# Optimization experiments

Measured on AMD Instinct MI355X. Metric: run time of the kernel, lower is better.

## Reference

```python
import jax, jax.numpy as jnp
import numpy as np
from jax import lax

IN, H, L, NC = 1024, 256, 3, 8
B, T = 64, 512


def setup_inputs() -> dict:
    key = jax.random.key(0)
    ks = iter(jax.random.split(key, 32))
    def u(shape, fan_in):
        s = 1.0 / np.sqrt(fan_in)
        return jax.random.uniform(next(ks), shape, jnp.float32, -s, s)
    inp = {"x": jax.random.normal(next(ks), (B, T, IN), jnp.float32)}
    dims = [IN, H, H]
    for l in range(L):
        inp[f"Wih{l}"] = u((4 * H, dims[l]), H)
        inp[f"Whh{l}"] = u((4 * H, H), H)
        # combined bias b_ih + b_hh (mathematically identical)
        inp[f"b{l}"] = u((4 * H,), H) + u((4 * H,), H)
    inp["W1"] = u((128, H), H)
    inp["bfc1"] = u((128,), H)
    inp["W2"] = u((NC, 128), 128)
    inp["bfc2"] = u((NC,), 128)
    return inp


def _lstm_layer(x_tbd, Wih, Whh, b):
    # x_tbd: (T, B, D). Precompute input gates with one big GEMM.
    xg = jnp.einsum("tbd,gd->tbg", x_tbd, Wih) + b  # (T, B, 4H)
    h0 = jnp.zeros((x_tbd.shape[1], H), x_tbd.dtype)
    def step(carry, xg_t):
        h, c = carry
        g = xg_t + h @ Whh.T
        i, f, gg, o = jnp.split(g, 4, axis=-1)  # torch gate order i,f,g,o
        i, f, o = jax.nn.sigmoid(i), jax.nn.sigmoid(f), jax.nn.sigmoid(o)
        c = f * c + i * jnp.tanh(gg)
        h = o * jnp.tanh(c)
        return (h, c), h
    _, hs = lax.scan(step, (h0, h0), xg)
    return hs  # (T, B, H)


def reference(x, Wih0, Whh0, b0, Wih1, Whh1, b1, Wih2, Whh2, b2, W1, bfc1, W2, bfc2):
    h = jnp.transpose(x, (1, 0, 2))  # (T, B, IN)
    for Wih, Whh, b in ((Wih0, Whh0, b0), (Wih1, Whh1, b1), (Wih2, Whh2, b2)):
        h = _lstm_layer(h, Wih, Whh, b)
    last = h[-1]  # (B, H) output at final timestep
    z = jax.nn.relu(last @ W1.T + bfc1)
    return z @ W2.T + bfc2  # (B, NC)
```

## Files before the change

### kernel.cpp

```cpp
#include <hip/hip_runtime.h>
#include <hip/hip_cooperative_groups.h>
#include <cmath>

namespace cg = cooperative_groups;

#define IN_DIM 1024
#define HD 256
#define G4H 1024
#define BB 64
#define TT 512
#define NCLS 8

#define SLOT_STRIDE (HD * BB)
#define LAYER_STRIDE (4 * SLOT_STRIDE)

__device__ __forceinline__ float sigmoidf_(float x) {
    return 1.0f / (1.0f + __expf(-x));
}
__device__ __forceinline__ float tanhf_(float x) {
    return 2.0f / (1.0f + __expf(-2.0f * x)) - 1.0f;
}
__device__ __forceinline__ unsigned long long ld_agent_u64(const unsigned long long* p) {
    return __hip_atomic_load(p, __ATOMIC_RELAXED, __HIP_MEMORY_SCOPE_AGENT);
}
__device__ __forceinline__ void st_agent_u64(unsigned long long* p, unsigned long long v) {
    __hip_atomic_store(p, v, __ATOMIC_RELAXED, __HIP_MEMORY_SCOPE_AGENT);
}

#define GBM 128
#define GBN 128
#define GBK 16

__global__ __launch_bounds__(256) void xg0_gemm(const float* __restrict__ x,
                                                const float* __restrict__ Wih0,
                                                const float* __restrict__ b0,
                                                float* __restrict__ xg0T) {
    __shared__ float As[GBK][GBM];
    __shared__ float Bs[GBK][GBN];
    const int m0 = blockIdx.y * GBM;
    const int n0 = blockIdx.x * GBN;
    const int tid = threadIdx.x;
    const int tx = tid & 15;
    const int ty = tid >> 4;
    const int lr = tid >> 1;
    const int lk = (tid & 1) * 8;
    const int am = m0 + lr;
    const size_t arow = (size_t)(am & 63) * TT + (am >> 6);
    float acc[8][8] = {};
    for (int k0 = 0; k0 < IN_DIM; k0 += GBK) {
        const float4 a0 = *(const float4*)&x[arow * IN_DIM + k0 + lk];
        const float4 a1 = *(const float4*)&x[arow * IN_DIM + k0 + lk + 4];
        const float4 w0 = *(const float4*)&Wih0[(size_t)(n0 + lr) * IN_DIM + k0 + lk];
        const float4 w1 = *(const float4*)&Wih0[(size_t)(n0 + lr) * IN_DIM + k0 + lk + 4];
        __syncthreads();
        As[lk + 0][lr] = a0.x; As[lk + 1][lr] = a0.y; As[lk + 2][lr] = a0.z; As[lk + 3][lr] = a0.w;
        As[lk + 4][lr] = a1.x; As[lk + 5][lr] = a1.y; As[lk + 6][lr] = a1.z; As[lk + 7][lr] = a1.w;
        Bs[lk + 0][lr] = w0.x; Bs[lk + 1][lr] = w0.y; Bs[lk + 2][lr] = w0.z; Bs[lk + 3][lr] = w0.w;
        Bs[lk + 4][lr] = w1.x; Bs[lk + 5][lr] = w1.y; Bs[lk + 6][lr] = w1.z; Bs[lk + 7][lr] = w1.w;
        __syncthreads();
#pragma unroll
        for (int k = 0; k < GBK; ++k) {
            const float4 av0 = *(const float4*)&As[k][ty * 8];
            const float4 av1 = *(const float4*)&As[k][ty * 8 + 4];
            const float4 bv0 = *(const float4*)&Bs[k][tx * 8];
            const float4 bv1 = *(const float4*)&Bs[k][tx * 8 + 4];
            const float am8[8] = {av0.x, av0.y, av0.z, av0.w, av1.x, av1.y, av1.z, av1.w};
            const float bn8[8] = {bv0.x, bv0.y, bv0.z, bv0.w, bv1.x, bv1.y, bv1.z, bv1.w};
#pragma unroll
            for (int i = 0; i < 8; ++i)
#pragma unroll
                for (int jj = 0; jj < 8; ++jj)
                    acc[i][jj] = fmaf(am8[i], bn8[jj], acc[i][jj]);
        }
    }
    const float4 bias0 = *(const float4*)&b0[n0 + tx * 8];
    const float4 bias1 = *(const float4*)&b0[n0 + tx * 8 + 4];
    const float bia[8] = {bias0.x, bias0.y, bias0.z, bias0.w, bias1.x, bias1.y, bias1.z, bias1.w};
#pragma unroll
    for (int i = 0; i < 8; ++i) {
        const int m = m0 + ty * 8 + i;
        const int t = m >> 6;
        const int bb = m & 63;
#pragma unroll
        for (int jj = 0; jj < 8; ++jj) {
            const int n = n0 + tx * 8 + jj;
            xg0T[((size_t)t * G4H + n) * BB + bb] = acc[i][jj] + bia[jj];
        }
    }
}

__global__ __launch_bounds__(512) void lstm_cells(
    const float* __restrict__ xg0T,
    const float* __restrict__ Whh0,
    const float* __restrict__ Wih1, const float* __restrict__ Whh1, const float* __restrict__ b1,
    const float* __restrict__ Wih2, const float* __restrict__ Whh2, const float* __restrict__ b2,
    unsigned long long* __restrict__ ringU, int* __restrict__ flags)
{
    cg::grid_group grid = cg::this_grid();
    const int blk = blockIdx.x;
    const int layer = blk >> 6;
    const int lb = blk & 63;
    const int jbase = lb * 4;
    const int tid = threadIdx.x;
    const int w = tid >> 6;
    const int b = tid & 63;
    const int kbase = w * 32;

    __shared__ float red[16][8][64];
    __shared__ float wlds[2][16][256];

    const float* Wih = (layer == 1) ? Wih1 : Wih2;
    const float* Whh = (layer == 0) ? Whh0 : ((layer == 1) ? Whh1 : Whh2);
    const float* bias = (layer == 1) ? b1 : b2;

    for (int idx = tid; idx < 16 * 64; idx += 512) {
        const int r = idx >> 6;
        const int cc = (idx & 63) << 2;
        const int jl = r >> 2, g = r & 3;
        *(float4*)&wlds[0][r][cc] =
            *(const float4*)&Whh[(size_t)(g * HD + jbase + jl) * HD + cc];
        if (layer > 0)
            *(float4*)&wlds[1][r][cc] =
                *(const float4*)&Wih[(size_t)(g * HD + jbase + jl) * HD + cc];
    }

    for (int i = blk * 512 + tid; i < 3 * LAYER_STRIDE; i += 192 * 512) ringU[i] = 0ull;
    for (int i = blk * 512 + tid; i < 3 * TT * 64; i += 192 * 512) flags[i] = 0;

    float bs0 = 0.f, bs1 = 0.f, bs2 = 0.f, bs3 = 0.f;
    if (layer > 0 && tid < 256) {
        bs0 = bias[0 * HD + jbase + w]; bs1 = bias[1 * HD + jbase + w];
        bs2 = bias[2 * HD + jbase + w]; bs3 = bias[3 * HD + jbase + w];
    }

    unsigned long long* myU = ringU + (size_t)layer * LAYER_STRIDE;
    const unsigned long long* inU = ringU + (size_t)(layer - 1) * LAYER_STRIDE;

    float c = 0.0f;

    grid.sync();

    for (int t = 0; t < TT; ++t) {
        float xv0, xv1, xv2, xv3;
        if (layer == 0 && tid < 256) {
            const float* xg = xg0T + ((size_t)t * G4H + jbase + w) * BB + b;
            xv0 = xg[0 * HD * BB]; xv1 = xg[1 * HD * BB];
            xv2 = xg[2 * HD * BB]; xv3 = xg[3 * HD * BB];
        }
        __atomic_signal_fence(__ATOMIC_SEQ_CST);

        if (layer < 2 && t >= 4 && tid < 64) {
            const int* f_nxt = &flags[((layer + 1) * TT + (t - 4)) * 64 + tid];
            for (;;) {
                int ok = __hip_atomic_load(f_nxt, __ATOMIC_RELAXED, __HIP_MEMORY_SCOPE_AGENT);
                if (__all(ok)) break;
                __builtin_amdgcn_s_sleep(2);
            }
        }

        float hv[32];
        {
            const unsigned long long* hp = myU + (size_t)((t + 3) & 3) * SLOT_STRIDE
                                         + (size_t)kbase * BB + b;
            const unsigned want = (unsigned)t;
            unsigned long long v[32];
            for (;;) {
#pragma unroll
                for (int u = 0; u < 32; ++u) v[u] = ld_agent_u64(hp + (size_t)u * BB);
                unsigned ok = 1;
#pragma unroll
                for (int u = 0; u < 32; ++u) ok &= ((unsigned)(v[u] >> 32) == want) ? 1u : 0u;
                if (__all(ok != 0)) break;
                __builtin_amdgcn_s_sleep(2);
            }
#pragma unroll
            for (int u = 0; u < 32; ++u) hv[u] = __uint_as_float((unsigned)v[u]);
        }

        float gv[32];
        if (layer > 0) {
            const unsigned long long* gp = inU + (size_t)(t & 3) * SLOT_STRIDE
                                         + (size_t)kbase * BB + b;
            const unsigned want = (unsigned)(t + 1);
            unsigned long long v[32];
            for (;;) {
#pragma unroll
                for (int u = 0; u < 32; ++u) v[u] = ld_agent_u64(gp + (size_t)u * BB);
                unsigned ok = 1;
#pragma unroll
                for (int u = 0; u < 32; ++u) ok &= ((unsigned)(v[u] >> 32) == want) ? 1u : 0u;
                if (__all(ok != 0)) break;
                __builtin_amdgcn_s_sleep(2);
            }
#pragma unroll
            for (int u = 0; u < 32; ++u) gv[u] = __uint_as_float((unsigned)v[u]);
        }

        float acc[16];
#pragma unroll
        for (int r = 0; r < 16; ++r) {
            const float4* wr0 = (const float4*)&wlds[0][r][kbase];
            float a = 0.0f;
#pragma unroll
            for (int q = 0; q < 8; ++q) {
                const float4 wv = wr0[q];
                a = fmaf(wv.x, hv[4 * q + 0], a);
                a = fmaf(wv.y, hv[4 * q + 1], a);
                a = fmaf(wv.z, hv[4 * q + 2], a);
                a = fmaf(wv.w, hv[4 * q + 3], a);
            }
            if (layer > 0) {
                const float4* wr1 = (const float4*)&wlds[1][r][kbase];
#pragma unroll
                for (int q = 0; q < 8; ++q) {
                    const float4 wv = wr1[q];
                    a = fmaf(wv.x, gv[4 * q + 0], a);
                    a = fmaf(wv.y, gv[4 * q + 1], a);
                    a = fmaf(wv.z, gv[4 * q + 2], a);
                    a = fmaf(wv.w, gv[4 * q + 3], a);
                }
            }
            acc[r] = a;
        }

#pragma unroll
        for (int r = 0; r < 16; ++r) red[r][w][b] = acc[r];
        __syncthreads();

        if (tid == 0) {
            __hip_atomic_store(&flags[(layer * TT + t) * 64 + lb], 1,
                               __ATOMIC_RELAXED, __HIP_MEMORY_SCOPE_AGENT);
        }

        if (tid < 256) {
            float a0, a1, a2, a3;
            if (layer == 0) { a0 = xv0; a1 = xv1; a2 = xv2; a3 = xv3; }
            else            { a0 = bs0; a1 = bs1; a2 = bs2; a3 = bs3; }
#pragma unroll
            for (int ww = 0; ww < 8; ++ww) {
                a0 += red[w * 4 + 0][ww][b];
                a1 += red[w * 4 + 1][ww][b];
                a2 += red[w * 4 + 2][ww][b];
                a3 += red[w * 4 + 3][ww][b];
            }
            const float ig = sigmoidf_(a0);
            const float fg = sigmoidf_(a1);
            const float gg = tanhf_(a2);
            const float og = sigmoidf_(a3);
            c = fg * c + ig * gg;
            const float h = og * tanhf_(c);
            const unsigned long long pk =
                ((unsigned long long)(unsigned)(t + 1) << 32) |
                (unsigned long long)__float_as_uint(h);
            st_agent_u64(&myU[(size_t)(t & 3) * SLOT_STRIDE
                              + (size_t)(jbase + w) * BB + b], pk);
        }

        __syncthreads();
    }
}

__global__ __launch_bounds__(256) void classifier_k(
    const unsigned long long* __restrict__ ringU,
    const float* __restrict__ W1, const float* __restrict__ bfc1,
    const float* __restrict__ W2, const float* __restrict__ bfc2,
    float* __restrict__ out)
{
    __shared__ float z[BB * 128];
    const unsigned long long* h2T = ringU + 2 * LAYER_STRIDE
                                  + (size_t)((TT - 1) & 3) * SLOT_STRIDE;
    const int tid = threadIdx.x;
    for (int idx = tid; idx < BB * 128; idx += 256) {
        const int bb = idx >> 7;
        const int n = idx & 127;
        float acc = bfc1[n];
        const float* wr = W1 + (size_t)n * HD;
        for (int k = 0; k < HD; ++k) {
            const float hval = __uint_as_float((unsigned)h2T[(size_t)k * BB + bb]);
            acc = fmaf(hval, wr[k], acc);
        }
        z[bb * 128 + n] = fmaxf(acc, 0.0f);
    }
    __syncthreads();
    for (int idx = tid; idx < BB * NCLS; idx += 256) {
        const int bb = idx >> 3;
        const int n = idx & 7;
        float acc = bfc2[n];
        const float* zr = &z[bb * 128];
        const float* wr = W2 + (size_t)n * 128;
        for (int k = 0; k < 128; k += 4) {
            const float4 zv = *(const float4*)&zr[k];
            const float4 wv = *(const float4*)&wr[k];
            acc = fmaf(zv.x, wv.x, acc); acc = fmaf(zv.y, wv.y, acc);
            acc = fmaf(zv.z, wv.z, acc); acc = fmaf(zv.w, wv.w, acc);
        }
        out[idx] = acc;
    }
}

extern "C" void kernel_launch(void* const* d_in, const int* in_sizes, int n_in,
                              void* d_out, int out_size, void* d_ws, size_t ws_size,
                              hipStream_t stream) {
    const float* x    = (const float*)d_in[0];
    const float* Wih0 = (const float*)d_in[1];
    const float* Whh0 = (const float*)d_in[2];
    const float* b0   = (const float*)d_in[3];
    const float* Wih1 = (const float*)d_in[4];
    const float* Whh1 = (const float*)d_in[5];
    const float* b1   = (const float*)d_in[6];
    const float* Wih2 = (const float*)d_in[7];
    const float* Whh2 = (const float*)d_in[8];
    const float* b2   = (const float*)d_in[9];
    const float* W1   = (const float*)d_in[10];
    const float* bfc1 = (const float*)d_in[11];
    const float* W2   = (const float*)d_in[12];
    const float* bfc2 = (const float*)d_in[13];

    float* xg0T = (float*)d_ws;
    unsigned long long* ringU =
        (unsigned long long*)(xg0T + (size_t)BB * TT * G4H);
    int* flags = (int*)(ringU + 3 * LAYER_STRIDE);

    xg0_gemm<<<dim3(G4H / GBN, (BB * TT) / GBM), 256, 0, stream>>>(x, Wih0, b0, xg0T);

    const float* xgc = xg0T;
    unsigned long long* ru = ringU;
    int* fl = flags;
    void* args[] = {
        (void*)&xgc, (void*)&Whh0,
        (void*)&Wih1, (void*)&Whh1, (void*)&b1,
        (void*)&Wih2, (void*)&Whh2, (void*)&b2,
        (void*)&ru, (void*)&fl
    };
    hipLaunchCooperativeKernel((void*)lstm_cells, dim3(192), dim3(512), args, 0, stream);

    classifier_k<<<1, 256, 0, stream>>>(ringU, W1, bfc1, W2, bfc2, (float*)d_out);
}
```

Before: 6.909 ms.

## Keep recurrent weights in registers and broadcast them via readlane instead of LDS

Removes the shared-memory weight tile. Each lane now holds 8 weight values in registers, and in the inner loop the weights are broadcast with readlane into SGPRs as scalar operands of the FMAs. The aim is to drop the LDS reads of weights on the serial per-timestep critical path. In exchange it adds many readlane instructions (scalar-unit work and wait states), and the input-weight pass for layers above 0 is split into a second loop.

```diff
diff --git a/kernel.cpp b/kernel.cpp
--- a/kernel.cpp
+++ b/kernel.cpp
@@ -107,21 +107,31 @@
     const int kbase = w * 32;
 
     __shared__ float red[16][8][64];
-    __shared__ float wlds[2][16][256];
 
     const float* Wih = (layer == 1) ? Wih1 : Wih2;
     const float* Whh = (layer == 0) ? Whh0 : ((layer == 1) ? Whh1 : Whh2);
     const float* bias = (layer == 1) ? b1 : b2;
 
-    for (int idx = tid; idx < 16 * 64; idx += 512) {
-        const int r = idx >> 6;
-        const int cc = (idx & 63) << 2;
-        const int jl = r >> 2, g = r & 3;
-        *(float4*)&wlds[0][r][cc] =
-            *(const float4*)&Whh[(size_t)(g * HD + jbase + jl) * HD + cc];
-        if (layer > 0)
-            *(float4*)&wlds[1][r][cc] =
-                *(const float4*)&Wih[(size_t)(g * HD + jbase + jl) * HD + cc];
+    float whreg[8];
+    float wihreg[8];
+    {
+        const int r = b >> 2;
+        const int jl = r >> 2;
+        const int g = r & 3;
+        const int kofs = kbase + (b & 3) * 8;
+        const float4 h0 = *(const float4*)&Whh[(size_t)(g * HD + jbase + jl) * HD + kofs];
+        const float4 h1 = *(const float4*)&Whh[(size_t)(g * HD + jbase + jl) * HD + kofs + 4];
+        whreg[0] = h0.x; whreg[1] = h0.y; whreg[2] = h0.z; whreg[3] = h0.w;
+        whreg[4] = h1.x; whreg[5] = h1.y; whreg[6] = h1.z; whreg[7] = h1.w;
+        if (layer > 0) {
+            const float4 i0 = *(const float4*)&Wih[(size_t)(g * HD + jbase + jl) * HD + kofs];
+            const float4 i1 = *(const float4*)&Wih[(size_t)(g * HD + jbase + jl) * HD + kofs + 4];
+            wihreg[0] = i0.x; wihreg[1] = i0.y; wihreg[2] = i0.z; wihreg[3] = i0.w;
+            wihreg[4] = i1.x; wihreg[5] = i1.y; wihreg[6] = i1.z; wihreg[7] = i1.w;
+        } else {
+#pragma unroll
+            for (int u = 0; u < 8; ++u) wihreg[u] = 0.0f;
+        }
     }
 
     for (int i = blk * 512 + tid; i < 3 * LAYER_STRIDE; i += 192 * 512) ringU[i] = 0ull;
@@ -199,28 +209,33 @@
         float acc[16];
 #pragma unroll
         for (int r = 0; r < 16; ++r) {
-            const float4* wr0 = (const float4*)&wlds[0][r][kbase];
             float a = 0.0f;
 #pragma unroll
-            for (int q = 0; q < 8; ++q) {
-                const float4 wv = wr0[q];
-                a = fmaf(wv.x, hv[4 * q + 0], a);
-                a = fmaf(wv.y, hv[4 * q + 1], a);
-                a = fmaf(wv.z, hv[4 * q + 2], a);
-                a = fmaf(wv.w, hv[4 * q + 3], a);
-            }
-            if (layer > 0) {
-                const float4* wr1 = (const float4*)&wlds[1][r][kbase];
-#pragma unroll
-                for (int q = 0; q < 8; ++q) {
-                    const float4 wv = wr1[q];
-                    a = fmaf(wv.x, gv[4 * q + 0], a);
-                    a = fmaf(wv.y, gv[4 * q + 1], a);
-                    a = fmaf(wv.z, gv[4 * q + 2], a);
-                    a = fmaf(wv.w, gv[4 * q + 3], a);
+            for (int q = 0; q < 4; ++q) {
+#pragma unroll
+                for (int u = 0; u < 8; ++u) {
+                    const float ws = __uint_as_float(
+                        __builtin_amdgcn_readlane(__float_as_uint(whreg[u]), r * 4 + q));
+                    a = fmaf(ws, hv[q * 8 + u], a);
                 }
             }
             acc[r] = a;
+        }
+        if (layer > 0) {
+#pragma unroll
+            for (int r = 0; r < 16; ++r) {
+                float a = acc[r];
+#pragma unroll
+                for (int q = 0; q < 4; ++q) {
+#pragma unroll
+                    for (int u = 0; u < 8; ++u) {
+                        const float ws = __uint_as_float(
+                            __builtin_amdgcn_readlane(__float_as_uint(wihreg[u]), r * 4 + q));
+                        a = fmaf(ws, gv[q * 8 + u], a);
+                    }
+                }
+                acc[r] = a;
+            }
         }
 
 #pragma unroll
```

Measured after the change: 6.839 ms. About the same (-1.0%).
